# Kernel optimization log

Hardware: AMD Instinct MI355X
Metric: run time of the kernel (lower is better)

Reference implementation:

```python
import jax, jax.numpy as jnp
import numpy as np

B, T, D, H = 4096, 512, 5, 64
G = 4 * H  # i,f,g,o gates stacked (PyTorch order)
FC1, FC2 = 32, 1


def _uniform(key, shape, scale):
    return jax.random.uniform(key, shape, jnp.float32, -scale, scale)


def setup_inputs() -> dict:
    key = jax.random.key(0)
    ks = jax.random.split(key, 14)
    s = 1.0 / np.sqrt(H)  # torch LSTM/Linear init scale
    return {
        "x": jax.random.normal(ks[0], (B, T, D), jnp.float32),
        "W_ih0": _uniform(ks[1], (G, D), s),
        "W_hh0": _uniform(ks[2], (G, H), s),
        "b_ih0": _uniform(ks[3], (G,), s),
        "b_hh0": _uniform(ks[4], (G,), s),
        "W_ih1": _uniform(ks[5], (G, H), s),
        "W_hh1": _uniform(ks[6], (G, H), s),
        "b_ih1": _uniform(ks[7], (G,), s),
        "b_hh1": _uniform(ks[8], (G,), s),
        "W1": _uniform(ks[9], (FC1, H), s),
        "b1": _uniform(ks[10], (FC1,), s),
        "W2": _uniform(ks[11], (FC2, FC1), 1.0 / np.sqrt(FC1)),
        "b2": _uniform(ks[12], (FC2,), 1.0 / np.sqrt(FC1)),
    }


def lstm_layer(x, W_ih, W_hh, b_ih, b_hh):
    # x: [B,T,Din] -> (h_seq [B,T,H], h_T [B,H])
    b = x.shape[0]
    h = W_hh.shape[1]
    # precompute input contribution for all timesteps
    pre = jnp.einsum('btd,gd->btg', x, W_ih) + b_ih + b_hh  # [B,T,4H]

    def step(carry, xt):
        hs, cs = carry
        gates = xt + hs @ W_hh.T  # [B,4H]
        i, f, g, o = jnp.split(gates, 4, axis=-1)
        i = jax.nn.sigmoid(i)
        f = jax.nn.sigmoid(f)
        g = jnp.tanh(g)
        o = jax.nn.sigmoid(o)
        cs = f * cs + i * g
        hs = o * jnp.tanh(cs)
        return (hs, cs), hs

    h0 = jnp.zeros((b, h), x.dtype)
    (hT, cT), h_seq = jax.lax.scan(step, (h0, h0), jnp.swapaxes(pre, 0, 1))
    return jnp.swapaxes(h_seq, 0, 1), hT


def reference(x, W_ih0, W_hh0, b_ih0, b_hh0, W_ih1, W_hh1, b_ih1, b_hh1, W1, b1, W2, b2):
    # eval mode: dropout layers are identity
    h1_seq, _ = lstm_layer(x, W_ih0, W_hh0, b_ih0, b_hh0)
    _, h2_T = lstm_layer(h1_seq, W_ih1, W_hh1, b_ih1, b_hh1)  # h_n[-1]
    z = jax.nn.relu(h2_T @ W1.T + b1)  # [B,32]
    out = z @ W2.T + b2  # [B,1]
    return out.squeeze(-1)  # [B]
```

## Files before the change

kernel.cpp:

```cpp
#include <hip/hip_runtime.h>
#include <cstddef>

#define T_STEPS  512
#define D_IN     5
#define NB       16
#define NTHREADS 1024
#define LOG2E    1.4426950408889634f

typedef __attribute__((ext_vector_type(8))) short f16x8;
typedef __attribute__((ext_vector_type(4))) float f32x4;

#define MFMA_INIT(D, A, B, C) \
    asm("v_mfma_f32_16x16x32_f16 %0, %1, %2, %3" : "=&v"(D) : "a"(A), "v"(B), "v"(C))
#define MFMA_ACC(D, A, B) \
    asm("v_mfma_f32_16x16x32_f16 %0, %1, %2, %0" : "+v"(D) : "a"(A), "v"(B))

__device__ __forceinline__ short f2h(float f) {
    return (short)__builtin_bit_cast(unsigned short, (_Float16)f);
}

__device__ __forceinline__ float lstm_cell(const f32x4 acc, float& c) {
    const float tg = __builtin_amdgcn_exp2f(acc[2]);
    const float ui = __builtin_amdgcn_exp2f(-acc[0]);
    const float uf = __builtin_amdgcn_exp2f(-acc[1]);
    const float A  = 1.0f + uf;
    const float Bd = (1.0f + ui) * (1.0f + tg);
    const float r  = __builtin_amdgcn_rcpf(A * Bd);
    c = fmaf(c, Bd, (tg - 1.0f) * A) * r;
    const float ca = fminf(c * (2.0f * LOG2E), 126.0f);
    const float tc = __builtin_amdgcn_exp2f(ca);
    const float uo = __builtin_amdgcn_exp2f(-acc[3]);
    return (tc - 1.0f) * __builtin_amdgcn_rcpf((1.0f + uo) * (1.0f + tc));
}

__device__ __forceinline__ int hswz8(int n, int u) {
    return (((u >> 3) ^ (n & 7)) << 3) | (u & 7);
}

__global__ __launch_bounds__(NTHREADS, 4)
void lstm_stack_mfma12(const float* __restrict__ x,
                       const float* __restrict__ W_ih0,
                       const float* __restrict__ W_hh0,
                       const float* __restrict__ b_ih0,
                       const float* __restrict__ b_hh0,
                       const float* __restrict__ W_ih1,
                       const float* __restrict__ W_hh1,
                       const float* __restrict__ b_ih1,
                       const float* __restrict__ b_hh1,
                       const float* __restrict__ W1,
                       const float* __restrict__ b1,
                       const float* __restrict__ W2,
                       const float* __restrict__ b2,
                       float* __restrict__ out)
{
    __shared__ alignas(16) unsigned short h1b[2][NB][64];
    __shared__ alignas(16) unsigned short h2b[2][NB][64];
    __shared__ alignas(16) float h2f[NB][68];
    __shared__ alignas(16) float zb[NB][36];

    const int tid  = threadIdx.x;
    const int b0   = blockIdx.x * NB;
    const int w    = tid >> 6;
    const int lane = tid & 63;
    const int n16  = lane & 15;
    const int quad = lane >> 4;

    f16x8 aX;
    f16x8 a0[2];
    f16x8 a1h1[2];
    f16x8 a1h2[2];
    f32x4 bc0, bc1;
    float c0 = 0.f, c1 = 0.f;

    {
        const int u_a = w * 4 + (n16 >> 2);
        const int g_a = n16 & 3;
        const int r0  = g_a * 64 + u_a;
        const float sc = (g_a == 2) ? 2.0f * LOG2E : LOG2E;
        #pragma unroll
        for (int j = 0; j < 8; ++j) {
            const int k = quad * 8 + j;
            aX[j] = f2h(k < D_IN ? sc * W_ih0[r0 * D_IN + k] : 0.0f);
        }
        #pragma unroll
        for (int kt = 0; kt < 2; ++kt) {
            #pragma unroll
            for (int j = 0; j < 8; ++j) {
                const int kk = kt * 32 + quad * 8 + j;
                a0[kt][j]   = f2h(sc * W_hh0[r0 * 64 + kk]);
                a1h1[kt][j] = f2h(sc * W_ih1[r0 * 64 + kk]);
                a1h2[kt][j] = f2h(sc * W_hh1[r0 * 64 + kk]);
            }
        }
        const int u_b = w * 4 + quad;
        #pragma unroll
        for (int r = 0; r < 4; ++r) {
            const float scr = (r == 2) ? 2.0f * LOG2E : LOG2E;
            bc0[r] = scr * (b_ih0[r * 64 + u_b] + b_hh0[r * 64 + u_b]);
            bc1[r] = scr * (b_ih1[r * 64 + u_b] + b_hh1[r * 64 + u_b]);
        }
    }

    for (int i = tid; i < 2 * NB * 64; i += NTHREADS) (&h1b[0][0][0])[i] = 0;
    for (int i = tid; i < 2 * NB * 64; i += NTHREADS) (&h2b[0][0][0])[i] = 0;
    __syncthreads();

    const int u_c = w * 4 + quad;
    const int f0 = ((0 * 4 + quad) ^ (n16 & 7)) * 8;
    const int f1 = ((1 * 4 + quad) ^ (n16 & 7)) * 8;
    const int wo = hswz8(n16, u_c);

    const float* xrow = &x[(size_t)(b0 + n16) * T_STEPS * D_IN];
    f16x8 bxq = {0, 0, 0, 0, 0, 0, 0, 0};
    float xf[D_IN] = {0.f, 0.f, 0.f, 0.f, 0.f};

    f32x4 pacc0, pacc1;
    {
        f16x8 bx0 = {0, 0, 0, 0, 0, 0, 0, 0};
        if (quad == 0) {
            #pragma unroll
            for (int d = 0; d < D_IN; ++d) bx0[d] = f2h(xrow[d]);
            #pragma unroll
            for (int d = 0; d < D_IN; ++d) bxq[d] = f2h(xrow[D_IN + d]);
        }
        MFMA_INIT(pacc0, aX, bx0, bc0);
        pacc1 = bc1;
    }

    #pragma unroll 1
    for (int t = 0; t <= T_STEPS + 1; ++t) {
        const int p = t & 1, q = p ^ 1;

        if (quad == 0 && (t + 2) < T_STEPS) {
            const float* xp = xrow + (size_t)(t + 2) * D_IN;
            #pragma unroll
            for (int d = 0; d < D_IN; ++d) xf[d] = xp[d];
        }

        const unsigned short* h1r = &h1b[q][n16][0];
        const unsigned short* h2r = &h2b[q][n16][0];
        f16x8 bh1[2], bh2[2];
        bh1[0] = *reinterpret_cast<const f16x8*>(h1r + f0);
        bh1[1] = *reinterpret_cast<const f16x8*>(h1r + f1);
        bh2[0] = *reinterpret_cast<const f16x8*>(h2r + f0);
        bh2[1] = *reinterpret_cast<const f16x8*>(h2r + f1);

        f32x4 acc0, acc1;
        MFMA_INIT(acc0, a0[0],   bh1[0], pacc0);
        MFMA_ACC (acc0, a0[1],   bh1[1]);
        MFMA_INIT(acc1, a1h2[0], bh2[0], pacc1);
        MFMA_ACC (acc1, a1h2[1], bh2[1]);
        MFMA_INIT(pacc0, aX,      bxq,    bc0);
        MFMA_INIT(pacc1, a1h1[0], bh1[0], bc1);
        MFMA_ACC (pacc1, a1h1[1], bh1[1]);

        asm("s_nop 7\n\ts_nop 7" : "+v"(acc0));
        if (t < T_STEPS) {
            const float h = lstm_cell(acc0, c0);
            h1b[p][n16][wo] = (unsigned short)f2h(h);
        }
        asm("s_nop 7\n\ts_nop 7" : "+v"(acc1));
        if (t >= 2) {
            const float h = lstm_cell(acc1, c1);
            h2b[p][n16][wo] = (unsigned short)f2h(h);
            if (t == T_STEPS + 1) h2f[n16][u_c] = h;
        }
        if (quad == 0 && (t + 2) < T_STEPS) {
            #pragma unroll
            for (int d = 0; d < D_IN; ++d) bxq[d] = f2h(xf[d]);
        }
        __syncthreads();
    }

    if (tid < 512) {
        const int bb = tid >> 5;
        const int k  = tid & 31;
        float a = b1[k];
        #pragma unroll 16
        for (int j = 0; j < 64; ++j)
            a = fmaf(W1[k * 64 + j], h2f[bb][j], a);
        zb[bb][k] = fmaxf(a, 0.0f);
    }
    __syncthreads();
    if (tid < NB) {
        float a = b2[0];
        #pragma unroll
        for (int k = 0; k < 32; ++k) a = fmaf(W2[k], zb[tid][k], a);
        out[b0 + tid] = a;
    }
}

extern "C" void kernel_launch(void* const* d_in, const int* in_sizes, int n_in,
                              void* d_out, int out_size, void* d_ws, size_t ws_size,
                              hipStream_t stream) {
    (void)in_sizes; (void)n_in; (void)d_ws; (void)ws_size;
    const float* xp     = (const float*)d_in[0];
    const float* W_ih0  = (const float*)d_in[1];
    const float* W_hh0  = (const float*)d_in[2];
    const float* b_ih0  = (const float*)d_in[3];
    const float* b_hh0  = (const float*)d_in[4];
    const float* W_ih1  = (const float*)d_in[5];
    const float* W_hh1  = (const float*)d_in[6];
    const float* b_ih1  = (const float*)d_in[7];
    const float* b_hh1  = (const float*)d_in[8];
    const float* W1     = (const float*)d_in[9];
    const float* b1     = (const float*)d_in[10];
    const float* W2     = (const float*)d_in[11];
    const float* b2     = (const float*)d_in[12];
    float* outp = (float*)d_out;

    const int nblocks = out_size / NB;
    hipLaunchKernelGGL(lstm_stack_mfma12, dim3(nblocks), dim3(NTHREADS), 0, stream,
                       xp, W_ih0, W_hh0, b_ih0, b_hh0,
                       W_ih1, W_hh1, b_ih1, b_hh1,
                       W1, b1, W2, b2, outp);
}
```

Measured before the change: 520.9 us.

## Halve block size so each wave computes two gate tiles per step

Cuts the block from 16 to 8 waves, with each wave now owning two 16-unit gate tiles and issuing twice as many MFMAs and cell updates per timestep. This is meant to lower the cost of the per-step block barrier and let independent MFMA chains interleave, hiding MFMA latency without the hand-inserted s_nops. It also replaces the inline-asm MFMAs (which pinned weights in AGPRs) with compiler builtins, which lets the compiler schedule them. The trade-off is more registers per wave and more serial work per wave on each step of the recurrence.

```diff
diff --git a/kernel.cpp b/kernel.cpp
--- a/kernel.cpp
+++ b/kernel.cpp
@@ -4,20 +4,13 @@
 #define T_STEPS  512
 #define D_IN     5
 #define NB       16
-#define NTHREADS 1024
+#define NTHREADS 512
 #define LOG2E    1.4426950408889634f
 
-typedef __attribute__((ext_vector_type(8))) short f16x8;
-typedef __attribute__((ext_vector_type(4))) float f32x4;
-
-#define MFMA_INIT(D, A, B, C) \
-    asm("v_mfma_f32_16x16x32_f16 %0, %1, %2, %3" : "=&v"(D) : "a"(A), "v"(B), "v"(C))
-#define MFMA_ACC(D, A, B) \
-    asm("v_mfma_f32_16x16x32_f16 %0, %1, %2, %0" : "+v"(D) : "a"(A), "v"(B))
-
-__device__ __forceinline__ short f2h(float f) {
-    return (short)__builtin_bit_cast(unsigned short, (_Float16)f);
-}
+typedef _Float16 half8 __attribute__((ext_vector_type(8)));
+typedef float    f32x4 __attribute__((ext_vector_type(4)));
+
+#define MFMA(A, B, C) __builtin_amdgcn_mfma_f32_16x16x32_f16((A), (B), (C), 0, 0, 0)
 
 __device__ __forceinline__ float lstm_cell(const f32x4 acc, float& c) {
     const float tg = __builtin_amdgcn_exp2f(acc[2]);
@@ -37,8 +30,8 @@
     return (((u >> 3) ^ (n & 7)) << 3) | (u & 7);
 }
 
-__global__ __launch_bounds__(NTHREADS, 4)
-void lstm_stack_mfma12(const float* __restrict__ x,
+__global__ __launch_bounds__(NTHREADS, 2)
+void lstm_stack_mfma15(const float* __restrict__ x,
                        const float* __restrict__ W_ih0,
                        const float* __restrict__ W_hh0,
                        const float* __restrict__ b_ih0,
@@ -53,10 +46,10 @@
                        const float* __restrict__ b2,
                        float* __restrict__ out)
 {
-    __shared__ alignas(16) unsigned short h1b[2][NB][64];
-    __shared__ alignas(16) unsigned short h2b[2][NB][64];
-    __shared__ alignas(16) float h2f[NB][68];
-    __shared__ alignas(16) float zb[NB][36];
+    __shared__ _Float16 h1b[2][NB][64];
+    __shared__ _Float16 h2b[2][NB][64];
+    __shared__ float h2f[NB][68];
+    __shared__ float zb[NB][36];
 
     const int tid  = threadIdx.x;
     const int b0   = blockIdx.x * NB;
@@ -65,66 +58,76 @@
     const int n16  = lane & 15;
     const int quad = lane >> 4;
 
-    f16x8 aX;
-    f16x8 a0[2];
-    f16x8 a1h1[2];
-    f16x8 a1h2[2];
-    f32x4 bc0, bc1;
-    float c0 = 0.f, c1 = 0.f;
-
-    {
-        const int u_a = w * 4 + (n16 >> 2);
+    half8 aX[2];
+    half8 a0[2][2];
+    half8 a1h1[2][2];
+    half8 a1h2[2][2];
+    f32x4 bc0[2], bc1[2];
+    float c0[2] = {0.f, 0.f}, c1[2] = {0.f, 0.f};
+
+    #pragma unroll
+    for (int tt = 0; tt < 2; ++tt) {
+        const int Tt  = 2 * w + tt;
+        const int u_a = Tt * 4 + (n16 >> 2);
         const int g_a = n16 & 3;
         const int r0  = g_a * 64 + u_a;
         const float sc = (g_a == 2) ? 2.0f * LOG2E : LOG2E;
         #pragma unroll
         for (int j = 0; j < 8; ++j) {
             const int k = quad * 8 + j;
-            aX[j] = f2h(k < D_IN ? sc * W_ih0[r0 * D_IN + k] : 0.0f);
+            aX[tt][j] = (k < D_IN) ? (_Float16)(sc * W_ih0[r0 * D_IN + k])
+                                   : (_Float16)0.f;
         }
         #pragma unroll
         for (int kt = 0; kt < 2; ++kt) {
             #pragma unroll
             for (int j = 0; j < 8; ++j) {
                 const int kk = kt * 32 + quad * 8 + j;
-                a0[kt][j]   = f2h(sc * W_hh0[r0 * 64 + kk]);
-                a1h1[kt][j] = f2h(sc * W_ih1[r0 * 64 + kk]);
-                a1h2[kt][j] = f2h(sc * W_hh1[r0 * 64 + kk]);
+                a0[tt][kt][j]   = (_Float16)(sc * W_hh0[r0 * 64 + kk]);
+                a1h1[tt][kt][j] = (_Float16)(sc * W_ih1[r0 * 64 + kk]);
+                a1h2[tt][kt][j] = (_Float16)(sc * W_hh1[r0 * 64 + kk]);
             }
         }
-        const int u_b = w * 4 + quad;
+        const int u_b = Tt * 4 + quad;
         #pragma unroll
         for (int r = 0; r < 4; ++r) {
             const float scr = (r == 2) ? 2.0f * LOG2E : LOG2E;
-            bc0[r] = scr * (b_ih0[r * 64 + u_b] + b_hh0[r * 64 + u_b]);
-            bc1[r] = scr * (b_ih1[r * 64 + u_b] + b_hh1[r * 64 + u_b]);
-        }
-    }
-
-    for (int i = tid; i < 2 * NB * 64; i += NTHREADS) (&h1b[0][0][0])[i] = 0;
-    for (int i = tid; i < 2 * NB * 64; i += NTHREADS) (&h2b[0][0][0])[i] = 0;
+            bc0[tt][r] = scr * (b_ih0[r * 64 + u_b] + b_hh0[r * 64 + u_b]);
+            bc1[tt][r] = scr * (b_ih1[r * 64 + u_b] + b_hh1[r * 64 + u_b]);
+        }
+    }
+
+    for (int i = tid; i < 2 * NB * 64; i += NTHREADS) (&h1b[0][0][0])[i] = (_Float16)0.f;
+    for (int i = tid; i < 2 * NB * 64; i += NTHREADS) (&h2b[0][0][0])[i] = (_Float16)0.f;
     __syncthreads();
 
-    const int u_c = w * 4 + quad;
     const int f0 = ((0 * 4 + quad) ^ (n16 & 7)) * 8;
     const int f1 = ((1 * 4 + quad) ^ (n16 & 7)) * 8;
-    const int wo = hswz8(n16, u_c);
+    int uc[2], wo[2];
+    #pragma unroll
+    for (int tt = 0; tt < 2; ++tt) {
+        uc[tt] = (2 * w + tt) * 4 + quad;
+        wo[tt] = hswz8(n16, uc[tt]);
+    }
 
     const float* xrow = &x[(size_t)(b0 + n16) * T_STEPS * D_IN];
-    f16x8 bxq = {0, 0, 0, 0, 0, 0, 0, 0};
+    half8 bxq = {};
     float xf[D_IN] = {0.f, 0.f, 0.f, 0.f, 0.f};
 
-    f32x4 pacc0, pacc1;
+    f32x4 pacc0[2], pacc1[2];
     {
-        f16x8 bx0 = {0, 0, 0, 0, 0, 0, 0, 0};
+        half8 bx0 = {};
         if (quad == 0) {
             #pragma unroll
-            for (int d = 0; d < D_IN; ++d) bx0[d] = f2h(xrow[d]);
-            #pragma unroll
-            for (int d = 0; d < D_IN; ++d) bxq[d] = f2h(xrow[D_IN + d]);
-        }
-        MFMA_INIT(pacc0, aX, bx0, bc0);
-        pacc1 = bc1;
+            for (int d = 0; d < D_IN; ++d) bx0[d] = (_Float16)xrow[d];
+            #pragma unroll
+            for (int d = 0; d < D_IN; ++d) bxq[d] = (_Float16)xrow[D_IN + d];
+        }
+        #pragma unroll
+        for (int tt = 0; tt < 2; ++tt) {
+            pacc0[tt] = MFMA(aX[tt], bx0, bc0[tt]);
+            pacc1[tt] = bc1[tt];
+        }
     }
 
     #pragma unroll 1
@@ -137,42 +140,49 @@
             for (int d = 0; d < D_IN; ++d) xf[d] = xp[d];
         }
 
-        const unsigned short* h1r = &h1b[q][n16][0];
-        const unsigned short* h2r = &h2b[q][n16][0];
-        f16x8 bh1[2], bh2[2];
-        bh1[0] = *reinterpret_cast<const f16x8*>(h1r + f0);
-        bh1[1] = *reinterpret_cast<const f16x8*>(h1r + f1);
-        bh2[0] = *reinterpret_cast<const f16x8*>(h2r + f0);
-        bh2[1] = *reinterpret_cast<const f16x8*>(h2r + f1);
-
-        f32x4 acc0, acc1;
-        MFMA_INIT(acc0, a0[0],   bh1[0], pacc0);
-        MFMA_ACC (acc0, a0[1],   bh1[1]);
-        MFMA_INIT(acc1, a1h2[0], bh2[0], pacc1);
-        MFMA_ACC (acc1, a1h2[1], bh2[1]);
-        MFMA_INIT(pacc0, aX,      bxq,    bc0);
-        MFMA_INIT(pacc1, a1h1[0], bh1[0], bc1);
-        MFMA_ACC (pacc1, a1h1[1], bh1[1]);
-
-        asm("s_nop 7\n\ts_nop 7" : "+v"(acc0));
+        const _Float16* h1r = &h1b[q][n16][0];
+        const _Float16* h2r = &h2b[q][n16][0];
+        half8 bh1[2], bh2[2];
+        bh1[0] = *reinterpret_cast<const half8*>(h1r + f0);
+        bh1[1] = *reinterpret_cast<const half8*>(h1r + f1);
+        bh2[0] = *reinterpret_cast<const half8*>(h2r + f0);
+        bh2[1] = *reinterpret_cast<const half8*>(h2r + f1);
+
+        f32x4 acc0[2], acc1[2];
+        #pragma unroll
+        for (int tt = 0; tt < 2; ++tt) {
+            acc0[tt] = MFMA(a0[tt][0],   bh1[0], pacc0[tt]);
+            acc0[tt] = MFMA(a0[tt][1],   bh1[1], acc0[tt]);
+            acc1[tt] = MFMA(a1h2[tt][0], bh2[0], pacc1[tt]);
+            acc1[tt] = MFMA(a1h2[tt][1], bh2[1], acc1[tt]);
+            pacc0[tt] = MFMA(aX[tt],      bxq,    bc0[tt]);
+            pacc1[tt] = MFMA(a1h1[tt][0], bh1[0], bc1[tt]);
+            pacc1[tt] = MFMA(a1h1[tt][1], bh1[1], pacc1[tt]);
+        }
+
         if (t < T_STEPS) {
-            const float h = lstm_cell(acc0, c0);
-            h1b[p][n16][wo] = (unsigned short)f2h(h);
-        }
-        asm("s_nop 7\n\ts_nop 7" : "+v"(acc1));
+            #pragma unroll
+            for (int tt = 0; tt < 2; ++tt) {
+                const float h = lstm_cell(acc0[tt], c0[tt]);
+                h1b[p][n16][wo[tt]] = (_Float16)h;
+            }
+        }
         if (t >= 2) {
-            const float h = lstm_cell(acc1, c1);
-            h2b[p][n16][wo] = (unsigned short)f2h(h);
-            if (t == T_STEPS + 1) h2f[n16][u_c] = h;
+            #pragma unroll
+            for (int tt = 0; tt < 2; ++tt) {
+                const float h = lstm_cell(acc1[tt], c1[tt]);
+                h2b[p][n16][wo[tt]] = (_Float16)h;
+                if (t == T_STEPS + 1) h2f[n16][uc[tt]] = h;
+            }
         }
         if (quad == 0 && (t + 2) < T_STEPS) {
             #pragma unroll
-            for (int d = 0; d < D_IN; ++d) bxq[d] = f2h(xf[d]);
+            for (int d = 0; d < D_IN; ++d) bxq[d] = (_Float16)xf[d];
         }
         __syncthreads();
     }
 
-    if (tid < 512) {
+    {
         const int bb = tid >> 5;
         const int k  = tid & 31;
         float a = b1[k];
@@ -210,7 +220,7 @@
     float* outp = (float*)d_out;
 
     const int nblocks = out_size / NB;
-    hipLaunchKernelGGL(lstm_stack_mfma12, dim3(nblocks), dim3(NTHREADS), 0, stream,
+    hipLaunchKernelGGL(lstm_stack_mfma15, dim3(nblocks), dim3(NTHREADS), 0, stream,
                        xp, W_ih0, W_hh0, b_ih0, b_hh0,
                        W_ih1, W_hh1, b_ih1, b_hh1,
                        W1, b1, W2, b2, outp);
```

Result: slower. 580.7 us (+11.5%).
